# Optimization experiments

Measured on AMD Instinct MI355X. Metric: run time of the kernel, lower is better.

The kernel has to match this reference:

```python
import jax, jax.numpy as jnp
import numpy as np

HIDDEN = 2304
N_HEADS = 8
N_KV_HEADS = 4
HEAD_DIM = 256
SLIDING_WINDOW = 4096
QUERY_PRE_ATTN_SCALAR = 256.0
SOFTCAP = 50.0
ROPE_BASE = 10000.0


def setup_inputs() -> dict:
    key = jax.random.key(0)
    ks = jax.random.split(key, 6)
    B, S = 1, 4096
    scale = 0.02
    return {
        "hidden_states": jax.random.normal(ks[0], (B, S, HIDDEN), dtype=jnp.float32),
        "Wq": jax.random.normal(ks[1], (HIDDEN, N_HEADS * HEAD_DIM), dtype=jnp.float32) * scale,
        "Wk": jax.random.normal(ks[2], (HIDDEN, N_KV_HEADS * HEAD_DIM), dtype=jnp.float32) * scale,
        "Wv": jax.random.normal(ks[3], (HIDDEN, N_KV_HEADS * HEAD_DIM), dtype=jnp.float32) * scale,
        "Wo": jax.random.normal(ks[4], (N_HEADS * HEAD_DIM, HIDDEN), dtype=jnp.float32) * scale,
        "position_ids": jnp.arange(S, dtype=jnp.int64 if jax.config.jax_enable_x64 else jnp.int32)[None, :],
    }


def _rope_cos_sin(position_ids):
    # inv_freq: (head_dim//2,)
    inv_freq = 1.0 / (ROPE_BASE ** (jnp.arange(0, HEAD_DIM, 2, dtype=jnp.float32) / HEAD_DIM))
    freqs = position_ids.astype(jnp.float32)[..., None] * inv_freq[None, None, :]  # (B,S,hd/2)
    emb = jnp.concatenate([freqs, freqs], axis=-1)  # (B,S,hd)
    return jnp.cos(emb), jnp.sin(emb)


def _rotate_half(x):
    x1, x2 = jnp.split(x, 2, axis=-1)
    return jnp.concatenate([-x2, x1], axis=-1)


def reference(hidden_states, Wq, Wk, Wv, Wo, position_ids):
    B, S, _ = hidden_states.shape
    cos, sin = _rope_cos_sin(position_ids)  # (B,S,hd)
    cos = cos[:, None]  # (B,1,S,hd) broadcast over heads
    sin = sin[:, None]

    q = (hidden_states @ Wq).reshape(B, S, N_HEADS, HEAD_DIM).transpose(0, 2, 1, 3)
    k = (hidden_states @ Wk).reshape(B, S, N_KV_HEADS, HEAD_DIM).transpose(0, 2, 1, 3)
    v = (hidden_states @ Wv).reshape(B, S, N_KV_HEADS, HEAD_DIM).transpose(0, 2, 1, 3)

    q = q * cos + _rotate_half(q) * sin
    k = k * cos + _rotate_half(k) * sin

    # GQA: repeat kv heads to match query heads
    n_rep = N_HEADS // N_KV_HEADS
    k = jnp.repeat(k, n_rep, axis=1)  # (B,H,S,hd)
    v = jnp.repeat(v, n_rep, axis=1)

    scaling = QUERY_PRE_ATTN_SCALAR ** -0.5
    scores = jnp.einsum("bhqd,bhkd->bhqk", q, k) * scaling

    # attention logit softcapping
    scores = SOFTCAP * jnp.tanh(scores / SOFTCAP)

    # causal + sliding window mask
    qi = jnp.arange(S)[:, None]
    kj = jnp.arange(S)[None, :]
    mask = (kj <= qi) & (qi - kj < SLIDING_WINDOW)  # (S,S)
    scores = jnp.where(mask[None, None], scores, jnp.asarray(-1e30, scores.dtype))

    attn = jax.nn.softmax(scores, axis=-1)
    ctx = jnp.einsum("bhqk,bhkd->bhqd", attn, v)  # (B,H,S,hd)
    ctx = ctx.transpose(0, 2, 1, 3).reshape(B, S, N_HEADS * HEAD_DIM)
    return ctx @ Wo
```

## Files before the change

### kernel.cpp

```cpp
#include <hip/hip_runtime.h>
#include <cstdint>
#include <cstddef>

typedef unsigned short u16;
typedef short bf16x8 __attribute__((ext_vector_type(8)));
typedef float f32x4 __attribute__((ext_vector_type(4)));

#define S_LEN 4096
#define HID   2304
#define NH    8
#define NKV   4
#define HD    256
#define QD    2048
#define KD    1024
#define QKVW  4096
#define CHT   32
#define SLOTS_PER_HEAD 160

__device__ __forceinline__ u16 f2b(float f) {
    union { float f; uint32_t u; } v; v.f = f;
    uint32_t r = (v.u + 0x7FFFu + ((v.u >> 16) & 1u)) >> 16;
    return (u16)r;
}
__device__ __forceinline__ float b2f(u16 u) {
    union { uint32_t u; float f; } v; v.u = ((uint32_t)u) << 16;
    return v.f;
}

__device__ __forceinline__ void glds16(const void* g, void* l) {
    __builtin_amdgcn_global_load_lds(
        (__attribute__((address_space(1))) void*)(const_cast<void*>(g)),
        (__attribute__((address_space(3))) void*)l, 16, 0, 0);
}

__device__ __forceinline__ int slot_base(int qt) {
    int a = qt >> 4, b = qt & 15;
    return (a + 1) * (8 * a + b);
}

__device__ __forceinline__ float softcap_p(float s) {
    float u = s * 0.00125f;
    u = fminf(fmaxf(u, -0.53f), 0.53f);
    float u2 = u * u;
    float t50 = u * (50.0f + u2 * (-16.6666667f + 6.66666667f * u2));
    return __expf(t50);
}

__global__ __launch_bounds__(256) void cvt_h(const float* __restrict__ in, u16* __restrict__ out, int n4) {
    int id = blockIdx.x * 256 + threadIdx.x;
    if (id >= n4) return;
    float4 v = ((const float4*)in)[id];
    uint2 o;
    o.x = (uint32_t)f2b(v.x) | ((uint32_t)f2b(v.y) << 16);
    o.y = (uint32_t)f2b(v.z) | ((uint32_t)f2b(v.w) << 16);
    ((uint2*)out)[id] = o;
}

__device__ __forceinline__ void twcvt_body(const float* __restrict__ W, u16* __restrict__ out,
                                           int K, int N, int ldo, int n0, int k0) {
    __shared__ float T[64][68];
    const int t = threadIdx.x;
    for (int i = 0; i < 4; i++) {
        int id = i * 256 + t;
        int r = id >> 4, c4 = id & 15;
        float4 v = *(const float4*)(W + (size_t)(k0 + r) * N + n0 + c4 * 4);
        *(float4*)(&T[r][c4 * 4]) = v;
    }
    __syncthreads();
    for (int i = 0; i < 4; i++) {
        int id = i * 256 + t;
        int rn = id >> 4, c4 = id & 15;
        u16 a = f2b(T[c4 * 4 + 0][rn]);
        u16 b = f2b(T[c4 * 4 + 1][rn]);
        u16 c = f2b(T[c4 * 4 + 2][rn]);
        u16 d = f2b(T[c4 * 4 + 3][rn]);
        uint2 o;
        o.x = (uint32_t)a | ((uint32_t)b << 16);
        o.y = (uint32_t)c | ((uint32_t)d << 16);
        *(uint2*)(out + (size_t)(n0 + rn) * ldo + k0 + c4 * 4) = o;
    }
}

__global__ __launch_bounds__(256) void twcvt(const float* __restrict__ W, u16* __restrict__ out,
                                             int K, int N, int ldo) {
    twcvt_body(W, out, K, N, ldo, blockIdx.x * 64, blockIdx.y * 64);
}

__global__ __launch_bounds__(256) void twcvt_qkv(const float* __restrict__ Wq,
                                                 const float* __restrict__ Wk,
                                                 const float* __restrict__ Wv,
                                                 u16* __restrict__ out) {
    const int z = blockIdx.z;
    const float* W = (z == 0) ? Wq : (z == 1) ? Wk : Wv;
    const int N = (z == 0) ? QD : KD;
    const int n0 = blockIdx.x * 64;
    if (n0 >= N) return;
    u16* ob = out + ((z == 0) ? 0 : (z == 1) ? (size_t)QD * HID : (size_t)(QD + KD) * HID);
    twcvt_body(W, ob, HID, N, HID, n0, blockIdx.y * 64);
}

template<int BF16_OUT>
__global__ __launch_bounds__(256, 2) void gemm_bt(const u16* __restrict__ A, const u16* __restrict__ B,
                                                  void* __restrict__ Cp, int M, int N, int K) {
    const int tid  = threadIdx.x;
    const int wv = tid >> 6, lane = tid & 63;
    const int quad = lane >> 4, m16 = lane & 15;
    const int gx = gridDim.x;
    int bid = blockIdx.y * gx + blockIdx.x;
    const int cpx = (gx * gridDim.y) >> 3;
    bid = (bid & 7) * cpx + (bid >> 3);
    const int m0 = (bid / gx) * 128, n0 = (bid % gx) * 128;
    const int wm = (wv & 1) * 64, wn = (wv >> 1) * 64;
    __shared__ __align__(16) u16 As[128 * 32];
    __shared__ __align__(16) u16 Bs[128 * 32];
    int s0i = (wv * 2) * 64 + lane, s1i = s0i + 64;
    int row0 = s0i >> 2, c0 = (s0i & 3) ^ (row0 & 3);
    int row1 = s1i >> 2, c1 = (s1i & 3) ^ (row1 & 3);
    const u16* pA0 = A + (size_t)(m0 + row0) * K + c0 * 8;
    const u16* pA1 = A + (size_t)(m0 + row1) * K + c1 * 8;
    const u16* pB0 = B + (size_t)(n0 + row0) * K + c0 * 8;
    const u16* pB1 = B + (size_t)(n0 + row1) * K + c1 * 8;
    u16* lA0 = &As[(wv * 2 + 0) * 512]; u16* lA1 = &As[(wv * 2 + 1) * 512];
    u16* lB0 = &Bs[(wv * 2 + 0) * 512]; u16* lB1 = &Bs[(wv * 2 + 1) * 512];

    const f32x4 z4 = {0.f, 0.f, 0.f, 0.f};
    f32x4 acc00 = z4, acc01 = z4, acc02 = z4, acc03 = z4;
    f32x4 acc10 = z4, acc11 = z4, acc12 = z4, acc13 = z4;
    f32x4 acc20 = z4, acc21 = z4, acc22 = z4, acc23 = z4;
    f32x4 acc30 = z4, acc31 = z4, acc32 = z4, acc33 = z4;

    const int sw = quad ^ (m16 & 3);
    const u16* ra0 = &As[(wm + 0 * 16 + m16) * 32 + (sw << 3)];
    const u16* ra1 = &As[(wm + 1 * 16 + m16) * 32 + (sw << 3)];
    const u16* ra2 = &As[(wm + 2 * 16 + m16) * 32 + (sw << 3)];
    const u16* ra3 = &As[(wm + 3 * 16 + m16) * 32 + (sw << 3)];
    const u16* rb0 = &Bs[(wn + 0 * 16 + m16) * 32 + (sw << 3)];
    const u16* rb1 = &Bs[(wn + 1 * 16 + m16) * 32 + (sw << 3)];
    const u16* rb2 = &Bs[(wn + 2 * 16 + m16) * 32 + (sw << 3)];
    const u16* rb3 = &Bs[(wn + 3 * 16 + m16) * 32 + (sw << 3)];

    for (int k0 = 0; k0 < K; k0 += 32) {
        __syncthreads();
        glds16(pA0 + k0, lA0);
        glds16(pA1 + k0, lA1);
        glds16(pB0 + k0, lB0);
        glds16(pB1 + k0, lB1);
        __syncthreads();
        bf16x8 af0 = *(const bf16x8*)ra0, af1 = *(const bf16x8*)ra1;
        bf16x8 af2 = *(const bf16x8*)ra2, af3 = *(const bf16x8*)ra3;
        bf16x8 bf0 = *(const bf16x8*)rb0, bf1 = *(const bf16x8*)rb1;
        bf16x8 bf2 = *(const bf16x8*)rb2, bf3 = *(const bf16x8*)rb3;
        acc00 = __builtin_amdgcn_mfma_f32_16x16x32_bf16(af0, bf0, acc00, 0, 0, 0);
        acc01 = __builtin_amdgcn_mfma_f32_16x16x32_bf16(af0, bf1, acc01, 0, 0, 0);
        acc02 = __builtin_amdgcn_mfma_f32_16x16x32_bf16(af0, bf2, acc02, 0, 0, 0);
        acc03 = __builtin_amdgcn_mfma_f32_16x16x32_bf16(af0, bf3, acc03, 0, 0, 0);
        acc10 = __builtin_amdgcn_mfma_f32_16x16x32_bf16(af1, bf0, acc10, 0, 0, 0);
        acc11 = __builtin_amdgcn_mfma_f32_16x16x32_bf16(af1, bf1, acc11, 0, 0, 0);
        acc12 = __builtin_amdgcn_mfma_f32_16x16x32_bf16(af1, bf2, acc12, 0, 0, 0);
        acc13 = __builtin_amdgcn_mfma_f32_16x16x32_bf16(af1, bf3, acc13, 0, 0, 0);
        acc20 = __builtin_amdgcn_mfma_f32_16x16x32_bf16(af2, bf0, acc20, 0, 0, 0);
        acc21 = __builtin_amdgcn_mfma_f32_16x16x32_bf16(af2, bf1, acc21, 0, 0, 0);
        acc22 = __builtin_amdgcn_mfma_f32_16x16x32_bf16(af2, bf2, acc22, 0, 0, 0);
        acc23 = __builtin_amdgcn_mfma_f32_16x16x32_bf16(af2, bf3, acc23, 0, 0, 0);
        acc30 = __builtin_amdgcn_mfma_f32_16x16x32_bf16(af3, bf0, acc30, 0, 0, 0);
        acc31 = __builtin_amdgcn_mfma_f32_16x16x32_bf16(af3, bf1, acc31, 0, 0, 0);
        acc32 = __builtin_amdgcn_mfma_f32_16x16x32_bf16(af3, bf2, acc32, 0, 0, 0);
        acc33 = __builtin_amdgcn_mfma_f32_16x16x32_bf16(af3, bf3, acc33, 0, 0, 0);
    }

#define STORE_TILE(I, J, ACC)                                              \
    {                                                                      \
        _Pragma("unroll")                                                  \
        for (int r = 0; r < 4; r++) {                                      \
            int row = m0 + wm + (I) * 16 + quad * 4 + r;                   \
            int col = n0 + wn + (J) * 16 + m16;                            \
            float v = (ACC)[r];                                            \
            if (BF16_OUT) ((u16*)Cp)[(size_t)row * N + col] = f2b(v);      \
            else          ((float*)Cp)[(size_t)row * N + col] = v;         \
        }                                                                  \
    }
    STORE_TILE(0, 0, acc00) STORE_TILE(0, 1, acc01) STORE_TILE(0, 2, acc02) STORE_TILE(0, 3, acc03)
    STORE_TILE(1, 0, acc10) STORE_TILE(1, 1, acc11) STORE_TILE(1, 2, acc12) STORE_TILE(1, 3, acc13)
    STORE_TILE(2, 0, acc20) STORE_TILE(2, 1, acc21) STORE_TILE(2, 2, acc22) STORE_TILE(2, 3, acc23)
    STORE_TILE(3, 0, acc30) STORE_TILE(3, 1, acc31) STORE_TILE(3, 2, acc32) STORE_TILE(3, 3, acc33)
#undef STORE_TILE
}

__global__ __launch_bounds__(256) void rope_k(const u16* __restrict__ QKV, const int* __restrict__ pos,
                                              u16* __restrict__ Qb, u16* __restrict__ Kb) {
    int id = blockIdx.x * 256 + threadIdx.x;
    const int NQ = S_LEN * NH * 128;
    const u16* src; u16* dst;
    int s, j;
    if (id < NQ) {
        s = id >> 10; int rem = id & 1023; int h = rem >> 7; j = rem & 127;
        src = QKV + (size_t)s * QKVW + h * 256;
        dst = Qb + (size_t)s * QD + h * 256;
    } else {
        int id2 = id - NQ;
        s = id2 >> 9; int rem = id2 & 511; int kvh = rem >> 7; j = rem & 127;
        src = QKV + (size_t)s * QKVW + QD + kvh * 256;
        dst = Kb + (size_t)s * KD + kvh * 256;
    }
    float p = (float)pos[s];
    float invf = expf(-0.07195578429985445f * (float)j);
    float ang = p * invf;
    float sn, cs;
    sincosf(ang, &sn, &cs);
    float x1 = b2f(src[j]), x2 = b2f(src[j + 128]);
    dst[j]       = f2b(x1 * cs - x2 * sn);
    dst[j + 128] = f2b(x2 * cs + x1 * sn);
}

__global__ __launch_bounds__(256) void vtrans(const u16* __restrict__ QKV, u16* __restrict__ Vt) {
    const int s0 = blockIdx.x * 64, d0 = blockIdx.y * 64;
    __shared__ u16 T[64][72];
    const int t = threadIdx.x;
    for (int i = 0; i < 2; i++) {
        int id = i * 256 + t;
        int r = id >> 3, c = id & 7;
        uint4 v = *(const uint4*)(QKV + (size_t)(s0 + r) * QKVW + (QD + KD) + d0 + c * 8);
        *(uint4*)(&T[r][c * 8]) = v;
    }
    __syncthreads();
    for (int i = 0; i < 2; i++) {
        int id = i * 256 + t;
        int r = id >> 3, c = id & 7;
        union { u16 u[8]; uint4 v; } o;
        for (int jj = 0; jj < 8; jj++) o.u[jj] = T[c * 8 + jj][r];
        *(uint4*)(Vt + (size_t)(d0 + r) * S_LEN + s0 + c * 8) = o.v;
    }
}

__global__ __launch_bounds__(256, 3) void attn_part(const u16* __restrict__ Qb, const u16* __restrict__ Kb,
                                                    const u16* __restrict__ Vt,
                                                    u16* __restrict__ Part, float* __restrict__ Lpart) {
    const int tid  = threadIdx.x;
    const int wv = tid >> 6, lane = tid & 63;
    const int quad = lane >> 4, m16 = lane & 15;
    const int qt = blockIdx.x, h = blockIdx.y, ch = blockIdx.z;
    const int n_kvt = 2 * qt + 2;
    const int t0 = ch * CHT;
    if (t0 >= n_kvt) return;
    const int t1 = min(t0 + CHT, n_kvt);
    const int kvh = h >> 1;
    const int q0 = qt * 64;
    const int slot = h * SLOTS_PER_HEAD + slot_base(qt) + ch;

    __shared__ __align__(16) u16 Kl[2][32 * 256];
    __shared__ __align__(16) u16 Vl[256 * 32];
    __shared__ __align__(16) u16 Pl[4][16 * 32];

    int kOff[4], vOff[4];
#pragma unroll
    for (int i = 0; i < 4; i++) {
        int s = (wv * 4 + i) * 64 + lane;
        int kv = s >> 5, c = (s & 31) ^ (kv & 7);
        kOff[i] = kv * KD + c * 8;
        int d = s >> 2, cc = (s & 3) ^ ((d >> 1) & 3);
        vOff[i] = d * S_LEN + cc * 8;
    }
    const u16* Kbase = Kb + kvh * 256;
    const u16* Vbase = Vt + (size_t)(kvh * 256) * S_LEN;

    bf16x8 qf[8];
    {
        const u16* qp = Qb + (size_t)(q0 + wv * 16 + m16) * QD + h * 256 + quad * 8;
#pragma unroll
        for (int ks = 0; ks < 8; ks++) qf[ks] = *(const bf16x8*)(qp + ks * 32);
    }
    float li[4] = {0.f, 0.f, 0.f, 0.f};
    f32x4 o[4][4];
#pragma unroll
    for (int i = 0; i < 4; i++)
#pragma unroll
        for (int j = 0; j < 4; j++) o[i][j] = (f32x4){0.f, 0.f, 0.f, 0.f};

#pragma unroll
    for (int i = 0; i < 4; i++)
        glds16(Kbase + kOff[i] + t0 * (32 * KD), &Kl[0][(wv * 4 + i) * 512]);

    for (int kt = t0; kt < t1; kt++) {
        const int cur = (kt - t0) & 1, nxt = cur ^ 1;
        asm volatile("s_waitcnt vmcnt(0)" ::: "memory");
        __builtin_amdgcn_sched_barrier(0);
        __builtin_amdgcn_s_barrier();
#pragma unroll
        for (int i = 0; i < 4; i++)
            glds16(Vbase + vOff[i] + kt * 32, &Vl[(wv * 4 + i) * 512]);
        if (kt + 1 < t1) {
#pragma unroll
            for (int i = 0; i < 4; i++)
                glds16(Kbase + kOff[i] + (kt + 1) * (32 * KD), &Kl[nxt][(wv * 4 + i) * 512]);
        }
        f32x4 s[2];
#pragma unroll
        for (int nt = 0; nt < 2; nt++) {
            f32x4 a = (f32x4){0.f, 0.f, 0.f, 0.f};
            int kr = nt * 16 + m16;
            int sw = kr & 7;
#pragma unroll
            for (int ks = 0; ks < 8; ks++) {
                int c = ks * 4 + quad;
                bf16x8 kf = *(const bf16x8*)(&Kl[cur][kr * 256 + ((c ^ sw) << 3)]);
                a = __builtin_amdgcn_mfma_f32_16x16x32_bf16(qf[ks], kf, a, 0, 0, 0);
            }
            s[nt] = a;
        }
        const int kvb = kt * 32;
        u16* Pw = &Pl[wv][0];
#pragma unroll
        for (int nt = 0; nt < 2; nt++)
#pragma unroll
            for (int r = 0; r < 4; r++) {
                float p = softcap_p(s[nt][r]);
                int kvg = kvb + nt * 16 + m16;
                int qg  = q0 + wv * 16 + quad * 4 + r;
                p = (kvg > qg) ? 0.f : p;
                li[r] += p;
                int m = quad * 4 + r;
                int c = 2 * nt + (m16 >> 3);
                int off = m16 & 7;
                Pw[m * 32 + ((c ^ ((m >> 1) & 3)) << 3) + off] = f2b(p);
            }
        if (kt + 1 < t1) {
            asm volatile("s_waitcnt vmcnt(4) lgkmcnt(0)" ::: "memory");
        } else {
            asm volatile("s_waitcnt vmcnt(0) lgkmcnt(0)" ::: "memory");
        }
        __builtin_amdgcn_sched_barrier(0);
        __builtin_amdgcn_s_barrier();
        bf16x8 pf[4];
#pragma unroll
        for (int qs = 0; qs < 4; qs++)
            pf[qs] = *(const bf16x8*)(&Pl[qs][m16 * 32 + ((quad ^ ((m16 >> 1) & 3)) << 3)]);
#pragma unroll
        for (int dt = 0; dt < 4; dt++) {
            int d = wv * 64 + dt * 16 + m16;
            bf16x8 vf = *(const bf16x8*)(&Vl[d * 32 + ((quad ^ ((d >> 1) & 3)) << 3)]);
            o[0][dt] = __builtin_amdgcn_mfma_f32_16x16x32_bf16(pf[0], vf, o[0][dt], 0, 0, 0);
            o[1][dt] = __builtin_amdgcn_mfma_f32_16x16x32_bf16(pf[1], vf, o[1][dt], 0, 0, 0);
            o[2][dt] = __builtin_amdgcn_mfma_f32_16x16x32_bf16(pf[2], vf, o[2][dt], 0, 0, 0);
            o[3][dt] = __builtin_amdgcn_mfma_f32_16x16x32_bf16(pf[3], vf, o[3][dt], 0, 0, 0);
        }
    }
    u16* Pp = Part + (size_t)slot * (64 * 256);
#pragma unroll
    for (int qs = 0; qs < 4; qs++)
#pragma unroll
        for (int dt = 0; dt < 4; dt++)
#pragma unroll
            for (int r = 0; r < 4; r++)
                Pp[(qs * 16 + quad * 4 + r) * 256 + wv * 64 + dt * 16 + m16] = f2b(o[qs][dt][r]);
#pragma unroll
    for (int r = 0; r < 4; r++) {
        float l = li[r];
        l += __shfl_xor(l, 1); l += __shfl_xor(l, 2);
        l += __shfl_xor(l, 4); l += __shfl_xor(l, 8);
        if (m16 == 0) Lpart[slot * 64 + wv * 16 + quad * 4 + r] = l;
    }
}

__global__ __launch_bounds__(256) void attn_combine(const u16* __restrict__ Part,
                                                    const float* __restrict__ Lpart,
                                                    u16* __restrict__ Ctx) {
    const int qt = blockIdx.x, h = blockIdx.y;
    const int nch = (qt >> 4) + 1;
    const int slot0 = h * SLOTS_PER_HEAD + slot_base(qt);
    const int t = threadIdx.x;
    const int q0 = qt * 64;
    __shared__ float linv[64];
    if (t < 64) {
        float l = 0.f;
        for (int c = 0; c < nch; c++) l += Lpart[(slot0 + c) * 64 + t];
        linv[t] = 1.f / l;
    }
    __syncthreads();
    const u16* P0 = Part + (size_t)slot0 * (64 * 256);
    for (int i = 0; i < 8; i++) {
        int idx = i * 256 + t;
        int row = idx >> 5, c8 = idx & 31;
        float acc[8] = {0.f,0.f,0.f,0.f,0.f,0.f,0.f,0.f};
        for (int c = 0; c < nch; c++) {
            uint4 v = *(const uint4*)(P0 + (size_t)c * (64 * 256) + row * 256 + c8 * 8);
            uint32_t w[4] = {v.x, v.y, v.z, v.w};
            for (int k = 0; k < 4; k++) {
                acc[k * 2]     += b2f((u16)(w[k] & 0xFFFF));
                acc[k * 2 + 1] += b2f((u16)(w[k] >> 16));
            }
        }
        float iv = linv[row];
        uint4 ov;
        uint32_t* op = (uint32_t*)&ov;
        for (int k = 0; k < 4; k++)
            op[k] = (uint32_t)f2b(acc[k * 2] * iv) | ((uint32_t)f2b(acc[k * 2 + 1] * iv) << 16);
        *(uint4*)(Ctx + (size_t)(q0 + row) * QD + h * 256 + c8 * 8) = ov;
    }
}

extern "C" void kernel_launch(void* const* d_in, const int* in_sizes, int n_in,
                              void* d_out, int out_size, void* d_ws, size_t ws_size,
                              hipStream_t stream) {
    const float* H  = (const float*)d_in[0];
    const float* Wq = (const float*)d_in[1];
    const float* Wk = (const float*)d_in[2];
    const float* Wv = (const float*)d_in[3];
    const float* Wo = (const float*)d_in[4];
    const int* pos  = (const int*)d_in[5];
    float* out = (float*)d_out;

    char* ws = (char*)d_ws;
    size_t off = 0;
    u16* Hb     = (u16*)(ws + off); off += (size_t)S_LEN * HID * 2;
    u16* Wqkvt  = (u16*)(ws + off); off += (size_t)QKVW * HID * 2;
    u16* Wot    = (u16*)(ws + off); off += (size_t)HID * QD * 2;
    u16* QKVraw = (u16*)(ws + off); off += (size_t)S_LEN * QKVW * 2;
    u16* Qb     = (u16*)(ws + off); off += (size_t)S_LEN * QD * 2;
    u16* Kb     = (u16*)(ws + off); off += (size_t)S_LEN * KD * 2;
    u16* Vt     = (u16*)(ws + off); off += (size_t)KD * S_LEN * 2;
    u16* Ctx    = (u16*)(ws + off); off += (size_t)S_LEN * QD * 2;
    u16* Part   = (u16*)(ws + off);  off += (size_t)NH * SLOTS_PER_HEAD * 64 * 256 * 2;
    float* Lprt = (float*)(ws + off); off += (size_t)NH * SLOTS_PER_HEAD * 64 * 4;

    cvt_h<<<dim3((S_LEN * HID / 4 + 255) / 256), dim3(256), 0, stream>>>(H, Hb, S_LEN * HID / 4);
    twcvt_qkv<<<dim3(32, HID / 64, 3), dim3(256), 0, stream>>>(Wq, Wk, Wv, Wqkvt);
    twcvt<<<dim3(HID / 64, QD / 64), dim3(256), 0, stream>>>(Wo, Wot, QD, HID, QD);
    gemm_bt<1><<<dim3(QKVW / 128, S_LEN / 128), dim3(256), 0, stream>>>(Hb, Wqkvt, QKVraw, S_LEN, QKVW, HID);
    rope_k<<<dim3((S_LEN * NH * 128 + S_LEN * NKV * 128) / 256), dim3(256), 0, stream>>>(QKVraw, pos, Qb, Kb);
    vtrans<<<dim3(S_LEN / 64, KD / 64), dim3(256), 0, stream>>>(QKVraw, Vt);
    attn_part<<<dim3(64, NH, 4), dim3(256), 0, stream>>>(Qb, Kb, Vt, Part, Lprt);
    attn_combine<<<dim3(64, NH), dim3(256), 0, stream>>>(Part, Lprt, Ctx);
    gemm_bt<0><<<dim3(HID / 128, S_LEN / 128), dim3(256), 0, stream>>>(Ctx, Wot, out, S_LEN, HID, QD);
}
```

Measured before the change: 454.7 us.

## Use 256x256 double-buffered 8-wave GEMM for QKV projection

Adds a new GEMM kernel with 256x256 output tiles, 512 threads and a K-step of 64. LDS is double-buffered, global-to-LDS prefetch of the next tile is interleaved with MFMA phases, and setprio is raised around MFMA bursts. The QKV projection now uses this kernel instead of the 128x128 one, aiming for more operand reuse per load and overlap of memory with compute. The grid shrinks to 256 blocks, which roughly matches the CU count, and 128 KB of LDS per block may limit occupancy to one block per CU.

```diff
diff --git a/kernel.cpp b/kernel.cpp
--- a/kernel.cpp
+++ b/kernel.cpp
@@ -97,6 +97,131 @@
     if (n0 >= N) return;
     u16* ob = out + ((z == 0) ? 0 : (z == 1) ? (size_t)QD * HID : (size_t)(QD + KD) * HID);
     twcvt_body(W, ob, HID, N, HID, n0, blockIdx.y * 64);
+}
+
+template<int BF16_OUT>
+__global__ __launch_bounds__(512, 2) void gemm256(const u16* __restrict__ A, const u16* __restrict__ B,
+                                                  void* __restrict__ Cp, int M, int N, int K) {
+    const int tid = threadIdx.x;
+    const int wv = tid >> 6, lane = tid & 63;
+    const int quad = lane >> 4, m16 = lane & 15;
+    const int gx = gridDim.x;
+    int bid = blockIdx.y * gx + blockIdx.x;
+    const int cpx = (gx * gridDim.y) >> 3;
+    bid = (bid & 7) * cpx + (bid >> 3);
+    const int m0 = (bid / gx) * 256, n0 = (bid % gx) * 256;
+    const int wm = (wv & 1) * 128, wn = (wv >> 1) * 64;
+
+    __shared__ __align__(16) u16 As[2][256 * 64];
+    __shared__ __align__(16) u16 Bs[2][256 * 64];
+
+    const int lr = lane >> 3, ls = lane & 7;
+    const int scol = ((ls ^ lr) << 3);
+    const u16* pA[4]; const u16* pB[4];
+    int du[4];
+#pragma unroll
+    for (int j = 0; j < 4; j++) {
+        int u = wv + 8 * j;
+        pA[j] = A + (size_t)(m0 + u * 8 + lr) * K + scol;
+        pB[j] = B + (size_t)(n0 + u * 8 + lr) * K + scol;
+        du[j] = u * 512;
+    }
+
+    f32x4 acc[8][4];
+#pragma unroll
+    for (int i = 0; i < 8; i++)
+#pragma unroll
+        for (int j = 0; j < 4; j++) acc[i][j] = (f32x4){0.f, 0.f, 0.f, 0.f};
+
+    const int aBase = (wm + m16) * 64;
+    const int bBase = (wn + m16) * 64;
+    const int s0 = ((quad ^ (m16 & 7)) << 3);
+    const int s1 = s0 ^ 32;
+
+    const int NT = K >> 6;
+#pragma unroll
+    for (int j = 0; j < 4; j++) glds16(pA[j], &As[0][du[j]]);
+#pragma unroll
+    for (int j = 0; j < 4; j++) glds16(pB[j], &Bs[0][du[j]]);
+    asm volatile("s_waitcnt vmcnt(0)" ::: "memory");
+    __builtin_amdgcn_sched_barrier(0);
+    __builtin_amdgcn_s_barrier();
+
+    for (int t = 0; t < NT; t++) {
+        const int cur = t & 1, nxt = cur ^ 1;
+        const int kn = (t + 1) << 6;
+        const bool pre = (t + 1 < NT);
+        bf16x8 af[4], bf[4];
+
+#define MFMA16(IOFF)                                                               \
+        _Pragma("unroll")                                                          \
+        for (int i = 0; i < 4; i++)                                                \
+            _Pragma("unroll")                                                      \
+            for (int j = 0; j < 4; j++)                                            \
+                acc[i + (IOFF)][j] =                                               \
+                    __builtin_amdgcn_mfma_f32_16x16x32_bf16(af[i], bf[j],          \
+                                                            acc[i + (IOFF)][j], 0, 0, 0);
+#define PHASE_SYNC()                                                               \
+        __builtin_amdgcn_s_barrier();                                              \
+        asm volatile("s_waitcnt lgkmcnt(0)" ::: "memory");                         \
+        __builtin_amdgcn_sched_barrier(0);
+
+#pragma unroll
+        for (int i = 0; i < 4; i++) af[i] = *(const bf16x8*)(&As[cur][aBase + i * 1024 + s0]);
+#pragma unroll
+        for (int j = 0; j < 4; j++) bf[j] = *(const bf16x8*)(&Bs[cur][bBase + j * 1024 + s0]);
+        if (pre) {
+#pragma unroll
+            for (int j = 0; j < 4; j++) glds16(pA[j] + kn, &As[nxt][du[j]]);
+        }
+        PHASE_SYNC();
+        __builtin_amdgcn_s_setprio(1);
+        MFMA16(0);
+        __builtin_amdgcn_s_setprio(0);
+        __builtin_amdgcn_s_barrier();
+#pragma unroll
+        for (int i = 0; i < 4; i++) af[i] = *(const bf16x8*)(&As[cur][aBase + (i + 4) * 1024 + s0]);
+        if (pre) {
+#pragma unroll
+            for (int j = 0; j < 4; j++) glds16(pB[j] + kn, &Bs[nxt][du[j]]);
+        }
+        PHASE_SYNC();
+        __builtin_amdgcn_s_setprio(1);
+        MFMA16(4);
+        __builtin_amdgcn_s_setprio(0);
+        __builtin_amdgcn_s_barrier();
+#pragma unroll
+        for (int i = 0; i < 4; i++) af[i] = *(const bf16x8*)(&As[cur][aBase + i * 1024 + s1]);
+#pragma unroll
+        for (int j = 0; j < 4; j++) bf[j] = *(const bf16x8*)(&Bs[cur][bBase + j * 1024 + s1]);
+        PHASE_SYNC();
+        __builtin_amdgcn_s_setprio(1);
+        MFMA16(0);
+        __builtin_amdgcn_s_setprio(0);
+        __builtin_amdgcn_s_barrier();
+#pragma unroll
+        for (int i = 0; i < 4; i++) af[i] = *(const bf16x8*)(&As[cur][aBase + (i + 4) * 1024 + s1]);
+        PHASE_SYNC();
+        __builtin_amdgcn_s_setprio(1);
+        MFMA16(4);
+        __builtin_amdgcn_s_setprio(0);
+        asm volatile("s_waitcnt vmcnt(0)" ::: "memory");
+        __builtin_amdgcn_sched_barrier(0);
+        __builtin_amdgcn_s_barrier();
+#undef MFMA16
+#undef PHASE_SYNC
+    }
+#pragma unroll
+    for (int i = 0; i < 8; i++)
+#pragma unroll
+        for (int j = 0; j < 4; j++)
+#pragma unroll
+            for (int r = 0; r < 4; r++) {
+                int row = m0 + wm + i * 16 + quad * 4 + r;
+                int col = n0 + wn + j * 16 + m16;
+                if (BF16_OUT) ((u16*)Cp)[(size_t)row * N + col] = f2b(acc[i][j][r]);
+                else          ((float*)Cp)[(size_t)row * N + col] = acc[i][j][r];
+            }
 }
 
 template<int BF16_OUT>
@@ -425,7 +550,7 @@
     cvt_h<<<dim3((S_LEN * HID / 4 + 255) / 256), dim3(256), 0, stream>>>(H, Hb, S_LEN * HID / 4);
     twcvt_qkv<<<dim3(32, HID / 64, 3), dim3(256), 0, stream>>>(Wq, Wk, Wv, Wqkvt);
     twcvt<<<dim3(HID / 64, QD / 64), dim3(256), 0, stream>>>(Wo, Wot, QD, HID, QD);
-    gemm_bt<1><<<dim3(QKVW / 128, S_LEN / 128), dim3(256), 0, stream>>>(Hb, Wqkvt, QKVraw, S_LEN, QKVW, HID);
+    gemm256<1><<<dim3(QKVW / 256, S_LEN / 256), dim3(512), 0, stream>>>(Hb, Wqkvt, QKVraw, S_LEN, QKVW, HID);
     rope_k<<<dim3((S_LEN * NH * 128 + S_LEN * NKV * 128) / 256), dim3(256), 0, stream>>>(QKVraw, pos, Qb, Kb);
     vtrans<<<dim3(S_LEN / 64, KD / 64), dim3(256), 0, stream>>>(QKVraw, Vt);
     attn_part<<<dim3(64, NH, 4), dim3(256), 0, stream>>>(Qb, Kb, Vt, Part, Lprt);
```

After: 447.0 us. No clear change (-1.7%).
